# Kernel optimization log

Measured on AMD Instinct MI355X. Metric: run time of the kernel, lower is better.

The kernel has to match this reference:

```python
import jax, jax.numpy as jnp
import numpy as np
from jax import lax

B, F_BINS, T = 4, 196, 1000
DM, H, DEPTH, FFN, L, EDIM = 512, 8, 64, 2048, 4, 128


def setup_inputs() -> dict:
    key = jax.random.key(0)
    ks = jax.random.split(key, 16)
    d = {}
    d['spec'] = jax.random.normal(ks[0], (B, 1, F_BINS, T), jnp.float32)
    d['conv1_w'] = jax.random.normal(ks[1], (32, 1, 5, 5), jnp.float32) / 5.0
    d['conv1_b'] = jax.random.normal(ks[2], (32,), jnp.float32) * 0.01
    d['conv2_w'] = jax.random.normal(ks[3], (64, 32, 5, 5), jnp.float32) / np.sqrt(32 * 25)
    d['conv2_b'] = jax.random.normal(ks[4], (64,), jnp.float32) * 0.01
    d['proj_w'] = jax.random.normal(ks[5], (DM, 64), jnp.float32) / 8.0
    d['proj_b'] = jnp.zeros((DM,), jnp.float32)
    d['ln1_g'] = jnp.ones((L, DM), jnp.float32)
    d['ln1_b'] = jnp.zeros((L, DM), jnp.float32)
    s = 1.0 / np.sqrt(DM)
    for i, nm in enumerate(['qw', 'kw', 'vw', 'dw']):
        d[nm] = jax.random.normal(ks[6 + i], (L, DM, DM), jnp.float32) * s
    for nm in ['qb', 'kb', 'vb', 'db']:
        d[nm] = jnp.zeros((L, DM), jnp.float32)
    d['Er'] = jax.random.normal(ks[10], (L, T, DEPTH), jnp.float32)
    d['ln2_g'] = jnp.ones((L, DM), jnp.float32)
    d['ln2_b'] = jnp.zeros((L, DM), jnp.float32)
    d['f1w'] = jax.random.normal(ks[11], (L, FFN, DM), jnp.float32) * s
    d['f1b'] = jnp.zeros((L, FFN), jnp.float32)
    d['f2w'] = jax.random.normal(ks[12], (L, DM, FFN), jnp.float32) / np.sqrt(FFN)
    d['f2b'] = jnp.zeros((L, DM), jnp.float32)
    d['deproj_w'] = jax.random.normal(ks[13], (EDIM, DM), jnp.float32) * s
    d['deproj_b'] = jnp.zeros((EDIM,), jnp.float32)
    return d


def _layernorm(x, g, b, eps=1e-5):
    mu = jnp.mean(x, -1, keepdims=True)
    var = jnp.mean(jnp.square(x - mu), -1, keepdims=True)
    return g * (x - mu) / jnp.sqrt(var + eps) + b


def _skew(QEr):
    # QEr: [B,H,S,S] -> music-transformer skew trick
    b, h, s, _ = QEr.shape
    padded = jnp.pad(QEr, ((0, 0), (0, 0), (0, 0), (1, 0)))  # [B,H,S,S+1]
    return padded.reshape(b, h, s + 1, s)[:, :, 1:, :]


def _forward(spec, conv1_w, conv1_b, conv2_w, conv2_b, proj_w, proj_b,
             ln1_g, ln1_b, qw, qb, kw, kb, vw, vb, dw, db, Er,
             ln2_g, ln2_b, f1w, f1b, f2w, f2b, deproj_w, deproj_b):
    dn = ('NCHW', 'OIHW', 'NCHW')
    x = lax.conv_general_dilated(spec, conv1_w, (1, 1), 'SAME', dimension_numbers=dn)
    x = jax.nn.gelu(x + conv1_b[None, :, None, None], approximate=False)
    x = lax.reduce_window(x, -jnp.inf, lax.max, (1, 1, 14, 1), (1, 1, 14, 1), 'VALID')
    x = lax.conv_general_dilated(x, conv2_w, (1, 1), 'SAME', dimension_numbers=dn)
    x = jax.nn.gelu(x + conv2_b[None, :, None, None], approximate=False)
    x = lax.reduce_window(x, -jnp.inf, lax.max, (1, 1, 14, 1), (1, 1, 14, 1), 'VALID')
    x = x.reshape(B, 64, T)              # freq collapsed to 1, flatten(1,2)
    x = x.transpose(0, 2, 1)             # [B,T,64]
    x = x @ proj_w.T + proj_b            # [B,T,DM]
    scale = 1.0 / np.sqrt(DEPTH)
    for l in range(L):
        xn = _layernorm(x, ln1_g[l], ln1_b[l])
        Q = (xn @ qw[l].T + qb[l]).reshape(B, T, H, DEPTH).transpose(0, 2, 1, 3)
        K = (xn @ kw[l].T + kb[l]).reshape(B, T, H, DEPTH).transpose(0, 2, 1, 3)
        V = (xn @ vw[l].T + vb[l]).reshape(B, T, H, DEPTH).transpose(0, 2, 1, 3)
        QEr = jnp.einsum('bhsd,rd->bhsr', Q, Er[l])        # relative pos scores
        Srel = _skew(QEr)
        logits = (jnp.einsum('bhsd,bhtd->bhst', Q, K) + Srel) * scale
        attn = jax.nn.softmax(logits, axis=-1)
        out = jnp.einsum('bhst,bhtd->bhsd', attn, V)
        out = out.transpose(0, 2, 1, 3).reshape(B, T, DM)
        x = x + (out @ dw[l].T + db[l])
        xn2 = _layernorm(x, ln2_g[l], ln2_b[l])
        ff = jax.nn.relu(xn2 @ f1w[l].T + f1b[l]) @ f2w[l].T + f2b[l]
        x = x + ff
    return x @ deproj_w.T + deproj_b     # [B,T,EDIM]


def reference(spec, conv1_w, conv1_b, conv2_w, conv2_b, proj_w, proj_b,
              ln1_g, ln1_b, qw, qb, kw, kb, vw, vb, dw, db, Er,
              ln2_g, ln2_b, f1w, f1b, f2w, f2b, deproj_w, deproj_b):
    return _forward(spec, conv1_w, conv1_b, conv2_w, conv2_b, proj_w, proj_b,
                    ln1_g, ln1_b, qw, qb, kw, kb, vw, vb, dw, db, Er,
                    ln2_g, ln2_b, f1w, f1b, f2w, f2b, deproj_w, deproj_b)
```

## Files before the change

### kernel.cpp

```cpp
#include <hip/hip_runtime.h>
#include <hip/hip_bf16.h>
#include <hip/hip_fp16.h>
#include <math.h>

#define BB 4
#define FBINS 196
#define TT 1000
#define DM 512
#define HH 8
#define DEPTH 64
#define FFN 2048
#define LL 4
#define EDIM 128
#define BT (BB*TT)
#define PSHIFT 12.0f

typedef __hip_bfloat16 bf16;
typedef __attribute__((ext_vector_type(8))) short short8;
typedef __attribute__((ext_vector_type(4))) float floatx4;

#define ARENA_BYTES 420000000ULL
static void* g_arena = nullptr;
__attribute__((constructor)) static void arena_init() {
    if (!g_arena) (void)hipMalloc(&g_arena, ARENA_BYTES);
}

__device__ __forceinline__ float gelu_f(float x) {
    return 0.5f * x * (1.0f + erff(x * 0.70710678118654752440f));
}

__global__ __launch_bounds__(256) void sniff_k(const unsigned short* __restrict__ p,
                                               int n, int* __restrict__ cnt) {
    int i = blockIdx.x * 256 + threadIdx.x;
    int c = 0;
    for (; i < n; i += gridDim.x * 256) {
        unsigned short u = p[i];
        if ((unsigned short)(u & 0x7FFF) > (unsigned short)0x7F80) c++;
    }
    if (c) atomicAdd(cnt, c);
}

#define NCVT 17
struct CvtArgs {
    const void* src[NCVT];
    unsigned dst[NCVT];
    unsigned cum[NCVT + 1];
    const int* cnt;
    float* dstA;
};
__global__ __launch_bounds__(256) void cvt_all(CvtArgs a) {
    unsigned i = blockIdx.x * 256 + threadIdx.x;
    if (i >= a.cum[NCVT]) return;
    bool isb = (*a.cnt == 0);
    int w = 0;
    while (i >= a.cum[w + 1]) w++;
    unsigned j = i - a.cum[w];
    float v = isb ? __bfloat162float(((const bf16*)a.src[w])[j])
                  : ((const float*)a.src[w])[j];
    a.dstA[a.dst[w] + j] = v;
}

__global__ __launch_bounds__(256) void f2bf_dyn(const void* __restrict__ src,
                                                bf16* __restrict__ d, int n,
                                                const int* __restrict__ cnt) {
    int i = blockIdx.x * 256 + threadIdx.x;
    if (i >= n) return;
    if (*cnt == 0) d[i] = ((const bf16*)src)[i];
    else           d[i] = __float2bfloat16(((const float*)src)[i]);
}

__global__ __launch_bounds__(256) void w2perm(const void* __restrict__ src,
                                              bf16* __restrict__ d,
                                              const int* __restrict__ cnt) {
    int idx = blockIdx.x * 256 + threadIdx.x;
    if (idx >= 51200) return;
    int c = idx / 800, k = idx - c * 800;
    int kc = k >> 5, ci = k & 31;
    int di = kc / 5, dj = kc - di * 5;
    int s = ((c * 32 + ci) * 5 + di) * 5 + dj;
    float v = (*cnt == 0) ? __bfloat162float(((const bf16*)src)[s])
                          : ((const float*)src)[s];
    d[idx] = __float2bfloat16(v);
}

__global__ __launch_bounds__(256) void conv1_pool2(const float* __restrict__ spec,
                                                   const float* __restrict__ w1,
                                                   const float* __restrict__ b1,
                                                   bf16* __restrict__ P1c) {
    __shared__ float ss[18][256];
    __shared__ float sw[200];
    int jt = blockIdx.x, p = blockIdx.y, z = blockIdx.z;
    int b = z >> 2, cg = z & 3;
    int tid = threadIdx.x;
    for (int i = tid; i < 200; i += 256) sw[i] = w1[cg * 200 + i];
    int ibase = p * 14, c0 = jt * 250 - 2;
    for (int idx = tid; idx < 18 * 256; idx += 256) {
        int rr = idx >> 8, cc = idx & 255;
        int gi = ibase - 2 + rr, gj = c0 + cc;
        ss[rr][cc] = (gi >= 0 && gi < FBINS && gj >= 0 && gj < TT && cc < 254)
                         ? spec[(size_t)b * FBINS * TT + (size_t)gi * TT + gj] : 0.f;
    }
    __syncthreads();
    if (tid >= 250) return;
    int j = jt * 250 + tid;
    unsigned short* orow = (unsigned short*)P1c + ((size_t)((b * 14 + p) * 1000 + j)) * 32;
    for (int cpl = 0; cpl < 8; cpl += 2) {
        int cp = cg * 8 + cpl;
        float conv[2][14];
        float b0 = b1[cp], b1v = b1[cp + 1];
#pragma unroll
        for (int i = 0; i < 14; i++) { conv[0][i] = b0; conv[1][i] = b1v; }
        const float* w0 = sw + cpl * 25;
        const float* w1p = sw + (cpl + 1) * 25;
        for (int rr = 0; rr < 18; rr++) {
            float v0 = ss[rr][tid], v1 = ss[rr][tid + 1], v2 = ss[rr][tid + 2],
                  v3 = ss[rr][tid + 3], v4 = ss[rr][tid + 4];
#pragma unroll
            for (int di = 0; di < 5; di++) {
                int i = rr - di;
                if (i >= 0 && i < 14) {
                    conv[0][i] += v0 * w0[di * 5] + v1 * w0[di * 5 + 1] + v2 * w0[di * 5 + 2]
                                + v3 * w0[di * 5 + 3] + v4 * w0[di * 5 + 4];
                    conv[1][i] += v0 * w1p[di * 5] + v1 * w1p[di * 5 + 1] + v2 * w1p[di * 5 + 2]
                                + v3 * w1p[di * 5 + 3] + v4 * w1p[di * 5 + 4];
                }
            }
        }
        float mx0 = -1e30f, mn0 = 1e30f, mx1 = -1e30f, mn1 = 1e30f;
#pragma unroll
        for (int i = 0; i < 14; i++) {
            mx0 = fmaxf(mx0, conv[0][i]); mn0 = fminf(mn0, conv[0][i]);
            mx1 = fmaxf(mx1, conv[1][i]); mn1 = fminf(mn1, conv[1][i]);
        }
        float m0 = fmaxf(gelu_f(mx0), gelu_f(mn0));
        float m1 = fmaxf(gelu_f(mx1), gelu_f(mn1));
        bf16 mb0 = __float2bfloat16(m0), mb1 = __float2bfloat16(m1);
        unsigned pk = ((unsigned)(*(unsigned short*)&mb1) << 16) |
                      (unsigned)(*(unsigned short*)&mb0);
        *(unsigned*)(orow + cp) = pk;
    }
}

__global__ __launch_bounds__(256) void conv2_gemm(const bf16* __restrict__ P1c,
                                                  const bf16* __restrict__ W2p,
                                                  const float* __restrict__ c2b,
                                                  bf16* __restrict__ convout) {
    __shared__ __align__(16) short Asm[64 * 40];
    __shared__ __align__(16) short Bsm[64 * 40];
    int tid = threadIdx.x, wave = tid >> 6, lane = tid & 63;
    int q = lane >> 4, l15 = lane & 15;
    int jt = blockIdx.x, i = blockIdx.y, b = blockIdx.z;
    int lrow = tid >> 2, lci = (tid & 3) * 8;
    int jrow = jt * 64 + lrow;
    int mw = (wave & 1) * 32, nw = (wave >> 1) * 32;
    floatx4 acc[2][2] = {};
    for (int di = 0; di < 5; di++) {
        int ii = i + di - 2;
        bool iok = (ii >= 0 && ii < 14);
        for (int dj = 0; dj < 5; dj++) {
            int kc = di * 5 + dj;
            {
                int jj = jrow + dj - 2;
                uint4 v = make_uint4(0u, 0u, 0u, 0u);
                if (iok && jrow < TT && jj >= 0 && jj < TT)
                    v = *(const uint4*)(P1c +
                        (((size_t)(b * 14 + ii)) * TT + jj) * 32 + lci);
                *(uint4*)(Asm + lrow * 40 + lci) = v;
            }
            {
                *(uint4*)(Bsm + lrow * 40 + lci) =
                    *(const uint4*)(W2p + (size_t)lrow * 800 + kc * 32 + lci);
            }
            __syncthreads();
            short8 a0 = *(const short8*)(Asm + (mw + l15) * 40 + q * 8);
            short8 a1 = *(const short8*)(Asm + (mw + 16 + l15) * 40 + q * 8);
            short8 b0 = *(const short8*)(Bsm + (nw + l15) * 40 + q * 8);
            short8 b1 = *(const short8*)(Bsm + (nw + 16 + l15) * 40 + q * 8);
            acc[0][0] = __builtin_amdgcn_mfma_f32_16x16x32_bf16(a0, b0, acc[0][0], 0, 0, 0);
            acc[0][1] = __builtin_amdgcn_mfma_f32_16x16x32_bf16(a0, b1, acc[0][1], 0, 0, 0);
            acc[1][0] = __builtin_amdgcn_mfma_f32_16x16x32_bf16(a1, b0, acc[1][0], 0, 0, 0);
            acc[1][1] = __builtin_amdgcn_mfma_f32_16x16x32_bf16(a1, b1, acc[1][1], 0, 0, 0);
            __syncthreads();
        }
    }
#pragma unroll
    for (int im = 0; im < 2; im++) {
#pragma unroll
        for (int jn = 0; jn < 2; jn++) {
            int c = nw + jn * 16 + l15;
            float bv = c2b[c];
#pragma unroll
            for (int r = 0; r < 4; r++) {
                int j = jt * 64 + mw + im * 16 + q * 4 + r;
                if (j >= TT) continue;
                convout[((size_t)(b * 14 + i) * TT + j) * 64 + c] =
                    __float2bfloat16(acc[im][jn][r] + bv);
            }
        }
    }
}

__global__ __launch_bounds__(256) void pool2_k(const bf16* __restrict__ convout,
                                               bf16* __restrict__ p2t) {
    int idx = blockIdx.x * 256 + threadIdx.x;
    if (idx >= 256000) return;
    int c = idx & 63, bj = idx >> 6;
    int b = bj / 1000, j = bj - b * 1000;
    float mx = -1e30f, mn = 1e30f;
#pragma unroll
    for (int i = 0; i < 14; i++) {
        float v = __bfloat162float(convout[((size_t)(b * 14 + i) * 1000 + j) * 64 + c]);
        mx = fmaxf(mx, v); mn = fminf(mn, v);
    }
    p2t[(size_t)bj * 64 + c] = __float2bfloat16(fmaxf(gelu_f(mx), gelu_f(mn)));
}

__global__ __launch_bounds__(256) void layernorm_k(const float* __restrict__ x,
                                                   const float* __restrict__ g,
                                                   const float* __restrict__ bta,
                                                   bf16* __restrict__ y) {
    __shared__ float red[256];
    int row = blockIdx.x, tid = threadIdx.x;
    const float* xr = x + (size_t)row * DM;
    float v0 = xr[tid], v1 = xr[tid + 256];
    red[tid] = v0 + v1;
    __syncthreads();
    for (int s = 128; s > 0; s >>= 1) { if (tid < s) red[tid] += red[tid + s]; __syncthreads(); }
    float mu = red[0] * (1.f / 512.f);
    __syncthreads();
    float d0 = v0 - mu, d1 = v1 - mu;
    red[tid] = d0 * d0 + d1 * d1;
    __syncthreads();
    for (int s = 128; s > 0; s >>= 1) { if (tid < s) red[tid] += red[tid + s]; __syncthreads(); }
    float rstd = rsqrtf(red[0] * (1.f / 512.f) + 1e-5f);
    bf16* yr = y + (size_t)row * DM;
    yr[tid]       = __float2bfloat16(d0 * rstd * g[tid]       + bta[tid]);
    yr[tid + 256] = __float2bfloat16(d1 * rstd * g[tid + 256] + bta[tid + 256]);
}

__global__ __launch_bounds__(256) void gemm_out(const float* __restrict__ A,
                                                const float* __restrict__ B,
                                                const float* __restrict__ bias,
                                                const int* __restrict__ cnt,
                                                void* __restrict__ dout,
                                                int M, int N, int K) {
    __shared__ float As[32][33];
    __shared__ float Bs[32][33];
    int tid = threadIdx.x;
    int tx = tid & 15, ty = tid >> 4;
    int m0 = blockIdx.x * 32, n0 = blockIdx.y * 32;
    float c[2][2] = {};
    for (int k0 = 0; k0 < K; k0 += 32) {
#pragma unroll
        for (int i = 0; i < 4; i++) {
            int idx = i * 256 + tid;
            int r = idx >> 5, kk = idx & 31;
            int gm = m0 + r;
            As[r][kk] = (gm < M) ? A[(size_t)gm * K + k0 + kk] : 0.f;
            Bs[r][kk] = B[(size_t)(n0 + r) * K + k0 + kk];
        }
        __syncthreads();
#pragma unroll
        for (int k = 0; k < 32; k++) {
            float a0 = As[ty * 2][k], a1 = As[ty * 2 + 1][k];
            float b0 = Bs[tx * 2][k], b1 = Bs[tx * 2 + 1][k];
            c[0][0] += a0 * b0; c[0][1] += a0 * b1;
            c[1][0] += a1 * b0; c[1][1] += a1 * b1;
        }
        __syncthreads();
    }
    bool isb = (*cnt == 0);
#pragma unroll
    for (int i = 0; i < 2; i++) {
        int m = m0 + ty * 2 + i;
        if (m >= M) continue;
#pragma unroll
        for (int jj = 0; jj < 2; jj++) {
            int n = n0 + tx * 2 + jj;
            float v = c[i][jj] + bias[n];
            if (isb) ((bf16*)dout)[(size_t)m * N + n] = __float2bfloat16(v);
            else     ((float*)dout)[(size_t)m * N + n] = v;
        }
    }
}

template <int BM, int NT, int ROUTE, int ACT, bool OUT_BF16>
__global__ __launch_bounds__(256) void mfma_big(const bf16* __restrict__ A,
                                                const bf16* __restrict__ B,
                                                const float* __restrict__ bias,
                                                const float* __restrict__ resid,
                                                float* __restrict__ Cf,
                                                bf16* __restrict__ Cb,
                                                int M, int N, int K,
                                                size_t wstride, int bstride,
                                                size_t ostride) {
    __shared__ __align__(16) short Asm[BM * 40];
    __shared__ __align__(16) short Bsm[NT * 40];
    int tid = threadIdx.x, wave = tid >> 6, lane = tid & 63;
    int q = lane >> 4, l15 = lane & 15;
    int m0 = blockIdx.x * BM, n0 = blockIdx.y * NT;
    int lrow = tid >> 2, lk = (tid & 3) * 8;
    constexpr int MF = (NT == 128) ? (BM / 16) : (BM / 32);
    int m0w = (NT == 128) ? 0 : ((wave >> 1) * (BM / 2));
    int nfb = (NT == 128) ? (wave * 32) : ((wave & 1) * 32);
    floatx4 acc[MF][2] = {};
    for (int k0 = 0; k0 < K; k0 += 32) {
#pragma unroll
        for (int hh = 0; hh < BM / 64; hh++) {
            int row = lrow + hh * 64, gm = m0 + row;
            uint4 v = make_uint4(0u, 0u, 0u, 0u);
            if (gm < M) v = *(const uint4*)(A + (size_t)gm * K + k0 + lk);
            *(uint4*)(Asm + row * 40 + lk) = v;
        }
#pragma unroll
        for (int hh = 0; hh < NT / 64; hh++) {
            int row = lrow + hh * 64, gn = n0 + row;
            const bf16* src = ROUTE
                ? B + (size_t)(gn >> 9) * wstride + (size_t)(gn & 511) * K + k0 + lk
                : B + (size_t)gn * K + k0 + lk;
            *(uint4*)(Bsm + row * 40 + lk) = *(const uint4*)src;
        }
        __syncthreads();
        short8 a[MF], b2[2];
#pragma unroll
        for (int im = 0; im < MF; im++)
            a[im] = *(const short8*)(Asm + (m0w + im * 16 + l15) * 40 + q * 8);
#pragma unroll
        for (int jn = 0; jn < 2; jn++)
            b2[jn] = *(const short8*)(Bsm + (nfb + jn * 16 + l15) * 40 + q * 8);
#pragma unroll
        for (int im = 0; im < MF; im++)
#pragma unroll
            for (int jn = 0; jn < 2; jn++)
                acc[im][jn] = __builtin_amdgcn_mfma_f32_16x16x32_bf16(
                    a[im], b2[jn], acc[im][jn], 0, 0, 0);
        __syncthreads();
    }
#pragma unroll
    for (int im = 0; im < MF; im++) {
#pragma unroll
        for (int jn = 0; jn < 2; jn++) {
            int nn = n0 + nfb + jn * 16 + l15;
            float bval = ROUTE ? bias[(nn >> 9) * bstride + (nn & 511)] : bias[nn];
#pragma unroll
            for (int r = 0; r < 4; r++) {
                int m = m0 + m0w + im * 16 + q * 4 + r;
                if (m >= M) continue;
                float v = acc[im][jn][r] + bval;
                if (resid) v += resid[(size_t)m * N + nn];
                if (ACT == 1) v = fmaxf(v, 0.f);
                if (ROUTE)
                    Cb[(size_t)(nn >> 9) * ostride + (size_t)m * 512 + (nn & 511)] =
                        __float2bfloat16(v);
                else if (OUT_BF16)
                    Cb[(size_t)m * N + nn] = __float2bfloat16(v);
                else
                    Cf[(size_t)m * N + nn] = v;
            }
        }
    }
}

__global__ __launch_bounds__(256) void vt_k(const bf16* __restrict__ Vb,
                                            bf16* __restrict__ Vt) {
    __shared__ short tile[64][65];
    int t0 = blockIdx.x * 64, z = blockIdx.y;
    int b = z >> 3, h = z & 7;
    int tid = threadIdx.x;
#pragma unroll
    for (int i = 0; i < 16; i++) {
        int tr = i * 4 + (tid >> 6), d = tid & 63;
        int t = t0 + tr;
        bf16 v = (t < TT) ? Vb[((size_t)b * TT + t) * DM + h * 64 + d] : (bf16)__float2bfloat16(0.f);
        tile[tr][d] = *(short*)&v;
    }
    __syncthreads();
#pragma unroll
    for (int i = 0; i < 16; i++) {
        int dr = i * 4 + (tid >> 6), tc = tid & 63;
        *(short*)&Vt[(size_t)z * 65536 + dr * 1024 + t0 + tc] = tile[tc][dr];
    }
}

__global__ __launch_bounds__(256, 2) void attn_fused(const bf16* __restrict__ Q,
                                                     const bf16* __restrict__ K,
                                                     const bf16* __restrict__ Er,
                                                     const bf16* __restrict__ Vt,
                                                     bf16* __restrict__ AO) {
    __shared__ __align__(16) short Qs[6400];
    __shared__ __align__(16) short pool[13000];
    __shared__ __align__(16) short Pl[64 * 136];
    __shared__ __align__(16) short Vs[64 * 136];
    __shared__ float rsw[4][64];
    int tid = threadIdx.x, wave = tid >> 6, lane = tid & 63;
    int q = lane >> 4, l15 = lane & 15;
    int m0 = blockIdx.x * 64;
    int z = blockIdx.z, b = z >> 3, h = z & 7;
    const bf16* Ap = Q + (size_t)b * TT * DM + h * 64;
    const bf16* Bp = K + (size_t)b * TT * DM + h * 64;
    const bf16* Vp = Vt + (size_t)z * 65536;
    int lrow = tid >> 2, lk = (tid & 3) * 8;
    int mw = wave * 16;

#pragma unroll
    for (int kh = 0; kh < 2; kh++) {
        int gm = m0 + lrow;
        uint4 v = make_uint4(0u, 0u, 0u, 0u);
        if (gm < TT) v = *(const uint4*)(Ap + (size_t)gm * DM + kh * 32 + lk);
        *(uint4*)(Qs + kh * 3200 + lrow * 40 + lk) = v;
        if (tid < 64) {
            int rr = 64 + (tid >> 2);
            int g2 = m0 + rr;
            uint4 v2 = make_uint4(0u, 0u, 0u, 0u);
            if (g2 < TT) v2 = *(const uint4*)(Ap + (size_t)g2 * DM + kh * 32 + lk);
            *(uint4*)(Qs + kh * 3200 + rr * 40 + lk) = v2;
        }
    }

    float rsum[16];
#pragma unroll
    for (int i = 0; i < 16; i++) rsum[i] = 0.f;
    floatx4 accO[4] = {};

    for (int tc = 0; tc < 8; tc++) {
        int t0 = tc * 128;
        int db = t0 - m0 - 64;
        floatx4 accS[4][2] = {};
        floatx4 accG[5][3] = {};
        for (int k0 = 0; k0 < 64; k0 += 32) {
            {
                int gn = t0 + lrow;
                uint4 v0 = make_uint4(0u, 0u, 0u, 0u), v1 = v0;
                if (gn < TT)      v0 = *(const uint4*)(Bp + (size_t)gn * DM + k0 + lk);
                if (gn + 64 < TT) v1 = *(const uint4*)(Bp + (size_t)(gn + 64) * DM + k0 + lk);
                *(uint4*)(pool + lrow * 40 + lk) = v0;
                *(uint4*)(pool + (lrow + 64) * 40 + lk) = v1;
            }
            {
#pragma unroll
                for (int hh = 0; hh < 3; hh++) {
                    int dd = lrow + hh * 64;
                    int dl = db + dd;
                    int src = (dl <= 0) ? (999 + dl) : (dl - 1);
                    uint4 v = make_uint4(0u, 0u, 0u, 0u);
                    if (src >= 0 && src < TT)
                        v = *(const uint4*)(Er + (size_t)src * 64 + k0 + lk);
                    *(uint4*)(pool + 5120 + dd * 40 + lk) = v;
                }
            }
            if (k0 == 0) {
#pragma unroll
                for (int e = 0; e < 4; e++) {
                    int li = tid + e * 256;
                    int row = li >> 4, cs = (li & 15) * 8;
                    *(uint4*)(Vs + row * 136 + cs) =
                        *(const uint4*)(Vp + (size_t)row * 1024 + t0 + cs);
                }
            }
            __syncthreads();
            short8 a[5], bk[2], e[3];
#pragma unroll
            for (int im = 0; im < 5; im++)
                a[im] = *(const short8*)(Qs + (k0 >> 5) * 3200 + (im * 16 + l15) * 40 + q * 8);
#pragma unroll
            for (int jn = 0; jn < 2; jn++)
                bk[jn] = *(const short8*)(pool + (wave * 32 + jn * 16 + l15) * 40 + q * 8);
#pragma unroll
            for (int jg = 0; jg < 3; jg++)
                e[jg] = *(const short8*)(pool + 5120 + (wave * 48 + jg * 16 + l15) * 40 + q * 8);
            __builtin_amdgcn_s_setprio(1);
#pragma unroll
            for (int im = 0; im < 4; im++)
#pragma unroll
                for (int jn = 0; jn < 2; jn++)
                    accS[im][jn] = __builtin_amdgcn_mfma_f32_16x16x32_bf16(
                        a[im], bk[jn], accS[im][jn], 0, 0, 0);
#pragma unroll
            for (int im = 0; im < 5; im++)
#pragma unroll
                for (int jg = 0; jg < 3; jg++)
                    accG[im][jg] = __builtin_amdgcn_mfma_f32_16x16x32_bf16(
                        a[im], e[jg], accG[im][jg], 0, 0, 0);
            __builtin_amdgcn_s_setprio(0);
            __syncthreads();
        }
#pragma unroll
        for (int im = 0; im < 5; im++)
#pragma unroll
            for (int jg = 0; jg < 3; jg++) {
                int col = wave * 48 + jg * 16 + l15;
#pragma unroll
                for (int r = 0; r < 4; r++) {
                    int row = im * 16 + q * 4 + r;
                    if (row < 65) {
                        bf16 gv = __float2bfloat16(accG[im][jg][r]);
                        pool[row * 200 + col] = *(short*)&gv;
                    }
                }
            }
        __syncthreads();
#pragma unroll
        for (int im = 0; im < 4; im++)
#pragma unroll
            for (int jn = 0; jn < 2; jn++) {
                int nl = wave * 32 + jn * 16 + l15;
                int n = t0 + nl;
#pragma unroll
                for (int r = 0; r < 4; r++) {
                    int ml = im * 16 + q * 4 + r;
                    int m = m0 + ml;
                    float pe = 0.f;
                    if (n < TT) {
                        float rel = 0.f;
                        if (n != m + 1) {
                            int u = (n <= m) ? m : (m + 1);
                            int dd = n - u - db;
                            short gs = pool[(u - m0) * 200 + dd];
                            rel = __bfloat162float(*(bf16*)&gs);
                        }
                        pe = __expf((accS[im][jn][r] + rel) * 0.125f - PSHIFT);
                        rsum[im * 4 + r] += pe;
                    }
                    bf16 pb = __float2bfloat16(pe);
                    Pl[ml * 136 + nl] = *(short*)&pb;
                }
            }
        __syncthreads();
        __builtin_amdgcn_s_setprio(1);
#pragma unroll
        for (int kc = 0; kc < 4; kc++) {
            short8 a = *(const short8*)(Pl + (mw + l15) * 136 + kc * 32 + q * 8);
#pragma unroll
            for (int jn = 0; jn < 4; jn++) {
                short8 bv = *(const short8*)(Vs + (jn * 16 + l15) * 136 + kc * 32 + q * 8);
                accO[jn] = __builtin_amdgcn_mfma_f32_16x16x32_bf16(a, bv, accO[jn], 0, 0, 0);
            }
        }
        __builtin_amdgcn_s_setprio(0);
        __syncthreads();
    }
#pragma unroll
    for (int t = 0; t < 16; t++) {
        float s = rsum[t];
        s += __shfl_xor(s, 1, 64); s += __shfl_xor(s, 2, 64);
        s += __shfl_xor(s, 4, 64); s += __shfl_xor(s, 8, 64);
        if (l15 == 0) rsw[wave][(t >> 2) * 16 + q * 4 + (t & 3)] = s;
    }
    __syncthreads();
#pragma unroll
    for (int r = 0; r < 4; r++) {
        int lm = mw + q * 4 + r;
        int m = m0 + lm;
        if (m >= TT) continue;
        float tot = rsw[0][lm] + rsw[1][lm] + rsw[2][lm] + rsw[3][lm];
        float inv = 1.f / tot;
#pragma unroll
        for (int jn = 0; jn < 4; jn++)
            AO[((size_t)b * TT + m) * DM + h * 64 + jn * 16 + l15] =
                __float2bfloat16(accO[jn][r] * inv);
    }
}

extern "C" void kernel_launch(void* const* d_in, const int* in_sizes, int n_in,
                              void* d_out, int out_size, void* d_ws, size_t ws_size,
                              hipStream_t stream) {
    if (!g_arena) (void)hipMalloc(&g_arena, ARENA_BYTES);
    float* A = (float*)g_arena;

    static const unsigned off[27] = {
        0, 784000, 784800, 784832, 836032, 836096, 868864, 869376, 871424,
        873472, 1922048, 2970624, 4019200, 5067776, 5069824, 5071872,
        5073920, 5075968, 5331968, 5334016, 5336064, 9530368, 9538560,
        13732864, 13734912, 13800448, 13800576};
    const float* spec  = A + off[0];
    const float* c1w   = A + off[1];
    const float* c1b   = A + off[2];
    const float* c2b   = A + off[4];
    const float* projb = A + off[6];
    const float* ln1g  = A + off[7];
    const float* ln1b  = A + off[8];
    const float* qb    = A + off[13];
    const float* db    = A + off[16];
    const float* ln2g  = A + off[18];
    const float* ln2b  = A + off[19];
    const float* f1b   = A + off[21];
    const float* f2b_  = A + off[23];
    const float* depw  = A + off[24];
    const float* depb  = A + off[25];

    const size_t PA = 13800576;
    float* x    = A + PA;
    float* P1   = x + 2048000;
    float* SM   = P1 + 1792000;
    bf16* P1c     = (bf16*)P1;
    bf16* p2t_b   = (bf16*)SM;
    bf16* projw_b = (bf16*)(SM + 128000);
    bf16* w2p     = (bf16*)(SM + 150000);
    int*   cnt  = (int*)(SM + 256000);
    float* ScF  = SM + 256004;
    float* B0   = ScF + 32000000;
    bf16* wb_qkvd = (bf16*)B0;
    bf16* wb_f1   = (bf16*)(B0 + 2097152);
    bf16* wb_f2   = (bf16*)(B0 + 4194304);
    bf16* Erb     = (bf16*)(B0 + 6291456);
    bf16* xn_b    = (bf16*)(B0 + 6419456);
    bf16* AO_b    = (bf16*)(B0 + 7443456);
    bf16* Qb_b    = (bf16*)(B0 + 8467456);
    bf16* Kb_b    = (bf16*)(B0 + 9491456);
    bf16* Vb_b    = (bf16*)(B0 + 10515456);
    bf16* FFH_b   = (bf16*)(B0 + 11539456);
    bf16* Vt      = (bf16*)(B0 + 15635456);
    bf16* convout = (bf16*)(B0 + 16684032);

    hipMemsetAsync(cnt, 0, sizeof(int), stream);
    sniff_k<<<1024, 256, 0, stream>>>((const unsigned short*)d_in[20], 1000000, cnt);

    static const int cvt_ids[NCVT] = {0, 1, 2, 4, 6, 7, 8, 13, 14, 15, 16,
                                      18, 19, 21, 23, 24, 25};
    CvtArgs ca;
    unsigned cum = 0;
    for (int t = 0; t < NCVT; t++) {
        int w = cvt_ids[t];
        ca.src[t] = d_in[w];
        ca.dst[t] = off[w];
        ca.cum[t] = cum;
        cum += off[w + 1] - off[w];
    }
    ca.cum[NCVT] = cum;
    ca.cnt = cnt; ca.dstA = A;
    cvt_all<<<(cum + 255) / 256, 256, 0, stream>>>(ca);

    for (int t = 0; t < 4; t++)
        f2bf_dyn<<<4096, 256, 0, stream>>>(d_in[9 + t], wb_qkvd + (size_t)t * 1048576,
                                           1048576, cnt);
    f2bf_dyn<<<16384, 256, 0, stream>>>(d_in[20], wb_f1, 4194304, cnt);
    f2bf_dyn<<<16384, 256, 0, stream>>>(d_in[22], wb_f2, 4194304, cnt);
    f2bf_dyn<<<1000,  256, 0, stream>>>(d_in[17], Erb,   256000, cnt);
    f2bf_dyn<<<128,   256, 0, stream>>>(d_in[5],  projw_b, 32768, cnt);
    w2perm<<<200, 256, 0, stream>>>(d_in[3], w2p, cnt);

    conv1_pool2<<<dim3(4, 14, 16), 256, 0, stream>>>(spec, c1w, c1b, P1c);
    conv2_gemm<<<dim3(16, 14, 4), 256, 0, stream>>>(P1c, w2p, c2b, convout);
    pool2_k<<<1000, 256, 0, stream>>>(convout, p2t_b);
    mfma_big<64, 64, 0, 0, false><<<dim3(63, 8), 256, 0, stream>>>(
        p2t_b, projw_b, projb, nullptr, x, nullptr, BT, DM, 64, 0, 0, 0);

    for (int l = 0; l < LL; l++) {
        layernorm_k<<<BT, 256, 0, stream>>>(x, ln1g + l * DM, ln1b + l * DM, xn_b);
        mfma_big<64, 128, 1, 0, true><<<dim3(63, 12), 256, 0, stream>>>(
            xn_b, wb_qkvd + (size_t)l * DM * DM, qb + l * DM, nullptr,
            nullptr, Qb_b, BT, 1536, DM, 1048576, 2048, 2048000);
        vt_k<<<dim3(16, 32), 256, 0, stream>>>(Vb_b, Vt);
        attn_fused<<<dim3(16, 1, 32), 256, 0, stream>>>(
            Qb_b, Kb_b, Erb + (size_t)l * TT * DEPTH, Vt, AO_b);
        mfma_big<64, 64, 0, 0, false><<<dim3(63, 8), 256, 0, stream>>>(
            AO_b, wb_qkvd + 3 * 1048576 + (size_t)l * DM * DM, db + l * DM, x,
            x, nullptr, BT, DM, DM, 0, 0, 0);
        layernorm_k<<<BT, 256, 0, stream>>>(x, ln2g + l * DM, ln2b + l * DM, xn_b);
        mfma_big<64, 128, 0, 1, true><<<dim3(63, 16), 256, 0, stream>>>(
            xn_b, wb_f1 + (size_t)l * FFN * DM, f1b + l * FFN, nullptr,
            nullptr, FFH_b, BT, FFN, DM, 0, 0, 0);
        mfma_big<64, 64, 0, 0, false><<<dim3(63, 8), 256, 0, stream>>>(
            FFH_b, wb_f2 + (size_t)l * DM * FFN, f2b_ + l * DM, x,
            x, nullptr, BT, DM, FFN, 0, 0, 0);
    }

    gemm_out<<<dim3(125, 4), 256, 0, stream>>>(x, depw, depb, cnt, d_out, BT, EDIM, DM);
}
```

Measured before the change: 1.089 ms.

## Halve attention key tile to 64 to shrink LDS and raise occupancy

The fused relative-position attention kernel now processes keys in 64-wide chunks instead of 128. The chunk loop runs 16 times instead of 8, and the K, Er, P and V shared buffers and accumulators shrink to match. Launch bounds move from 2 to 3 blocks per SM so more waves can be resident. In exchange there are twice as many barriers and loop iterations, and the relative-position (Er) band is recomputed with more overlap between neighbouring chunks.

Result: slower. 1.142 ms (+4.9%).

```diff
diff --git a/kernel.cpp b/kernel.cpp
--- a/kernel.cpp
+++ b/kernel.cpp
@@ -382,15 +382,15 @@
     }
 }
 
-__global__ __launch_bounds__(256, 2) void attn_fused(const bf16* __restrict__ Q,
+__global__ __launch_bounds__(256, 3) void attn_fused(const bf16* __restrict__ Q,
                                                      const bf16* __restrict__ K,
                                                      const bf16* __restrict__ Er,
                                                      const bf16* __restrict__ Vt,
                                                      bf16* __restrict__ AO) {
     __shared__ __align__(16) short Qs[6400];
-    __shared__ __align__(16) short pool[13000];
-    __shared__ __align__(16) short Pl[64 * 136];
-    __shared__ __align__(16) short Vs[64 * 136];
+    __shared__ __align__(16) short pool[8840];
+    __shared__ __align__(16) short Pl[64 * 72];
+    __shared__ __align__(16) short Vs[64 * 72];
     __shared__ float rsw[4][64];
     int tid = threadIdx.x, wave = tid >> 6, lane = tid & 63;
     int q = lane >> 4, l15 = lane & 15;
@@ -422,63 +422,57 @@
     for (int i = 0; i < 16; i++) rsum[i] = 0.f;
     floatx4 accO[4] = {};
 
-    for (int tc = 0; tc < 8; tc++) {
-        int t0 = tc * 128;
+    for (int tc = 0; tc < 16; tc++) {
+        int t0 = tc * 64;
         int db = t0 - m0 - 64;
-        floatx4 accS[4][2] = {};
-        floatx4 accG[5][3] = {};
+        floatx4 accS[4] = {};
+        floatx4 accG[5][2] = {};
         for (int k0 = 0; k0 < 64; k0 += 32) {
             {
                 int gn = t0 + lrow;
-                uint4 v0 = make_uint4(0u, 0u, 0u, 0u), v1 = v0;
-                if (gn < TT)      v0 = *(const uint4*)(Bp + (size_t)gn * DM + k0 + lk);
-                if (gn + 64 < TT) v1 = *(const uint4*)(Bp + (size_t)(gn + 64) * DM + k0 + lk);
-                *(uint4*)(pool + lrow * 40 + lk) = v0;
-                *(uint4*)(pool + (lrow + 64) * 40 + lk) = v1;
+                uint4 v = make_uint4(0u, 0u, 0u, 0u);
+                if (gn < TT) v = *(const uint4*)(Bp + (size_t)gn * DM + k0 + lk);
+                *(uint4*)(pool + lrow * 40 + lk) = v;
             }
             {
 #pragma unroll
-                for (int hh = 0; hh < 3; hh++) {
+                for (int hh = 0; hh < 2; hh++) {
                     int dd = lrow + hh * 64;
                     int dl = db + dd;
                     int src = (dl <= 0) ? (999 + dl) : (dl - 1);
                     uint4 v = make_uint4(0u, 0u, 0u, 0u);
                     if (src >= 0 && src < TT)
                         v = *(const uint4*)(Er + (size_t)src * 64 + k0 + lk);
-                    *(uint4*)(pool + 5120 + dd * 40 + lk) = v;
+                    *(uint4*)(pool + 2560 + dd * 40 + lk) = v;
                 }
             }
             if (k0 == 0) {
 #pragma unroll
-                for (int e = 0; e < 4; e++) {
-                    int li = tid + e * 256;
-                    int row = li >> 4, cs = (li & 15) * 8;
-                    *(uint4*)(Vs + row * 136 + cs) =
+                for (int e2 = 0; e2 < 2; e2++) {
+                    int li = tid + e2 * 256;
+                    int row = li >> 3, cs = (li & 7) * 8;
+                    *(uint4*)(Vs + row * 72 + cs) =
                         *(const uint4*)(Vp + (size_t)row * 1024 + t0 + cs);
                 }
             }
             __syncthreads();
-            short8 a[5], bk[2], e[3];
+            short8 a[5], bk, e[2];
 #pragma unroll
             for (int im = 0; im < 5; im++)
                 a[im] = *(const short8*)(Qs + (k0 >> 5) * 3200 + (im * 16 + l15) * 40 + q * 8);
-#pragma unroll
-            for (int jn = 0; jn < 2; jn++)
-                bk[jn] = *(const short8*)(pool + (wave * 32 + jn * 16 + l15) * 40 + q * 8);
-#pragma unroll
-            for (int jg = 0; jg < 3; jg++)
-                e[jg] = *(const short8*)(pool + 5120 + (wave * 48 + jg * 16 + l15) * 40 + q * 8);
+            bk = *(const short8*)(pool + (wave * 16 + l15) * 40 + q * 8);
+#pragma unroll
+            for (int jg = 0; jg < 2; jg++)
+                e[jg] = *(const short8*)(pool + 2560 + (wave * 32 + jg * 16 + l15) * 40 + q * 8);
             __builtin_amdgcn_s_setprio(1);
 #pragma unroll
             for (int im = 0; im < 4; im++)
-#pragma unroll
-                for (int jn = 0; jn < 2; jn++)
-                    accS[im][jn] = __builtin_amdgcn_mfma_f32_16x16x32_bf16(
-                        a[im], bk[jn], accS[im][jn], 0, 0, 0);
+                accS[im] = __builtin_amdgcn_mfma_f32_16x16x32_bf16(
+                    a[im], bk, accS[im], 0, 0, 0);
 #pragma unroll
             for (int im = 0; im < 5; im++)
 #pragma unroll
-                for (int jg = 0; jg < 3; jg++)
+                for (int jg = 0; jg < 2; jg++)
                     accG[im][jg] = __builtin_amdgcn_mfma_f32_16x16x32_bf16(
                         a[im], e[jg], accG[im][jg], 0, 0, 0);
             __builtin_amdgcn_s_setprio(0);
@@ -487,52 +481,50 @@
 #pragma unroll
         for (int im = 0; im < 5; im++)
 #pragma unroll
-            for (int jg = 0; jg < 3; jg++) {
-                int col = wave * 48 + jg * 16 + l15;
+            for (int jg = 0; jg < 2; jg++) {
+                int col = wave * 32 + jg * 16 + l15;
 #pragma unroll
                 for (int r = 0; r < 4; r++) {
                     int row = im * 16 + q * 4 + r;
                     if (row < 65) {
                         bf16 gv = __float2bfloat16(accG[im][jg][r]);
-                        pool[row * 200 + col] = *(short*)&gv;
+                        pool[row * 136 + col] = *(short*)&gv;
                     }
                 }
             }
         __syncthreads();
 #pragma unroll
-        for (int im = 0; im < 4; im++)
-#pragma unroll
-            for (int jn = 0; jn < 2; jn++) {
-                int nl = wave * 32 + jn * 16 + l15;
-                int n = t0 + nl;
-#pragma unroll
-                for (int r = 0; r < 4; r++) {
-                    int ml = im * 16 + q * 4 + r;
-                    int m = m0 + ml;
-                    float pe = 0.f;
-                    if (n < TT) {
-                        float rel = 0.f;
-                        if (n != m + 1) {
-                            int u = (n <= m) ? m : (m + 1);
-                            int dd = n - u - db;
-                            short gs = pool[(u - m0) * 200 + dd];
-                            rel = __bfloat162float(*(bf16*)&gs);
-                        }
-                        pe = __expf((accS[im][jn][r] + rel) * 0.125f - PSHIFT);
-                        rsum[im * 4 + r] += pe;
+        for (int im = 0; im < 4; im++) {
+            int nl = wave * 16 + l15;
+            int n = t0 + nl;
+#pragma unroll
+            for (int r = 0; r < 4; r++) {
+                int ml = im * 16 + q * 4 + r;
+                int m = m0 + ml;
+                float pe = 0.f;
+                if (n < TT) {
+                    float rel = 0.f;
+                    if (n != m + 1) {
+                        int ur = (n <= m) ? ml : (ml + 1);
+                        int dd = nl + 64 - ur;
+                        short gs = pool[ur * 136 + dd];
+                        rel = __bfloat162float(*(bf16*)&gs);
                     }
-                    bf16 pb = __float2bfloat16(pe);
-                    Pl[ml * 136 + nl] = *(short*)&pb;
+                    pe = __expf((accS[im][r] + rel) * 0.125f - PSHIFT);
+                    rsum[im * 4 + r] += pe;
                 }
-            }
+                bf16 pb = __float2bfloat16(pe);
+                Pl[ml * 72 + nl] = *(short*)&pb;
+            }
+        }
         __syncthreads();
         __builtin_amdgcn_s_setprio(1);
 #pragma unroll
-        for (int kc = 0; kc < 4; kc++) {
-            short8 a = *(const short8*)(Pl + (mw + l15) * 136 + kc * 32 + q * 8);
+        for (int kc = 0; kc < 2; kc++) {
+            short8 a = *(const short8*)(Pl + (mw + l15) * 72 + kc * 32 + q * 8);
 #pragma unroll
             for (int jn = 0; jn < 4; jn++) {
-                short8 bv = *(const short8*)(Vs + (jn * 16 + l15) * 136 + kc * 32 + q * 8);
+                short8 bv = *(const short8*)(Vs + (jn * 16 + l15) * 72 + kc * 32 + q * 8);
                 accO[jn] = __builtin_amdgcn_mfma_f32_16x16x32_bf16(a, bv, accO[jn], 0, 0, 0);
             }
         }
```
